# Kernel tuning notes

Measured on AMD Instinct MI355X. Metric: run time of the kernel, lower is better.

The kernel has to match this reference:

```python
import jax, jax.numpy as jnp
import numpy as np

B, C, T, F = 16, 2, 2000, 257

def setup_inputs() -> dict:
    key = jax.random.key(0)
    k1, = jax.random.split(key, 1)
    inp = jax.random.normal(k1, (B, C, T, F, 2), dtype=jnp.float32)
    s_1 = jnp.zeros((B, 1, F, 1), dtype=jnp.float32)
    weights = jnp.ones((1, C, 1, F, 1), dtype=jnp.float32)
    bias = jnp.zeros((1, C, 1, F, 1), dtype=jnp.float32)
    alpha_param = jnp.full((1, 1, F, 1), -4.0, dtype=jnp.float32)
    return {"input": inp, "s_1": s_1, "weights": weights, "bias": bias, "alpha_param": alpha_param}

def reference(input, s_1, weights, bias, alpha_param):
    # input: [B, C, T, F, 2]
    in_data2 = jnp.sum(input ** 2, axis=-1, keepdims=True)       # [B, C, T, F, 1]
    alpha = jax.nn.sigmoid(alpha_param)                           # [1, 1, F, 1]
    x_seq = jnp.moveaxis(in_data2[:, 0:1], 2, 0)                  # [T, B, 1, F, 1]

    def step(s, xt):
        s_new = s * (1.0 - alpha) + xt * alpha                    # [B, 1, F, 1]
        return s_new, s_new

    s_final, smooth = jax.lax.scan(step, s_1, x_seq)              # smooth: [T, B, 1, F, 1]
    smooth_data = jnp.sqrt(jnp.moveaxis(smooth, 0, 2))            # [B, 1, T, F, 1]
    cat_data = jnp.concatenate([smooth_data, jnp.sqrt(in_data2[:, 1:])], axis=1)  # [B, C, T, F, 1]
    res = input / (cat_data + 1e-8) * weights + bias              # [B, C, T, F, 2]
    return res, s_final, smooth_data
```

## Files before the change

### kernel.cpp

```cpp
#include <hip/hip_runtime.h>
#include <math.h>

#define B 16
#define C 2
#define T 2000
#define F 257
#define NC 100
#define L  (T / NC)

#define RES_SIZE   (B * C * T * F * 2)
#define OFF_SFINAL (RES_SIZE)
#define OFF_SMOOTH (RES_SIZE + B * F)

#define N_CARRY (B * NC * F)
#define G0      ((N_CARRY + 255) / 256)
#define SLAB4   (T * F * 2 / 4)
#define N_V4    (B * SLAB4)
#define G1      ((N_V4 + 255) / 256)

__device__ __forceinline__ float sigmoidf_(float x) {
    return 1.0f / (1.0f + expf(-x));
}

__global__ __launch_bounds__(256) void k_phase1(const float* __restrict__ input,
                                                const float* __restrict__ alpha_param,
                                                const float* __restrict__ weights,
                                                const float* __restrict__ bias,
                                                float* __restrict__ carry,
                                                float* __restrict__ out) {
    int bid = blockIdx.x;
    if (bid < G1) {
        int idx = bid * 256 + threadIdx.x;
        if (idx >= N_V4) return;
        int b   = idx / SLAB4;
        int rem = idx - b * SLAB4;

        const float4* ip = (const float4*)(input + ((size_t)(b * C + 1) * T) * F * 2) + rem;
        float4 v = *ip;

        int e  = rem * 2;
        int f0 = e % F;
        int f1 = (f0 + 1 == F) ? 0 : (f0 + 1);

        float w0 = weights[F + f0], w1 = weights[F + f1];
        float q0 = bias[F + f0],    q1 = bias[F + f1];

        float inv0 = 1.0f / (sqrtf(v.x * v.x + v.y * v.y) + 1e-8f);
        float inv1 = 1.0f / (sqrtf(v.z * v.z + v.w * v.w) + 1e-8f);

        float4 rr;
        rr.x = v.x * inv0 * w0 + q0;
        rr.y = v.y * inv0 * w0 + q0;
        rr.z = v.z * inv1 * w1 + q1;
        rr.w = v.w * inv1 * w1 + q1;

        float4* rp = (float4*)(out + ((size_t)(b * C + 1) * T) * F * 2) + rem;
        *rp = rr;
    } else {
        int tid = (bid - G1) * 256 + threadIdx.x;
        if (tid >= N_CARRY) return;
        int f = tid % F;
        int r = tid / F;
        int c = r % NC;
        int b = r / NC;

        float a = sigmoidf_(alpha_param[f]);
        float beta = 1.0f - a;

        const float2* inp = (const float2*)input
                          + ((size_t)(b * C + 0) * T + (size_t)c * L) * F + f;
        float s = 0.0f;
#pragma unroll
        for (int t = 0; t < L; ++t) {
            float2 v = inp[(size_t)t * F];
            s = beta * s + a * (v.x * v.x + v.y * v.y);
        }
        carry[((size_t)b * NC + c) * F + f] = s;
    }
}

__global__ __launch_bounds__(256) void k_phase2(const float* __restrict__ input,
                                                const float* __restrict__ s_1,
                                                const float* __restrict__ alpha_param,
                                                const float* __restrict__ weights,
                                                const float* __restrict__ bias,
                                                const float* __restrict__ carry,
                                                float* __restrict__ out) {
    int tid = blockIdx.x * 256 + threadIdx.x;
    if (tid >= N_CARRY) return;
    int f = tid % F;
    int r = tid / F;
    int c = r % NC;
    int b = r / NC;

    float a = sigmoidf_(alpha_param[f]);
    float beta = 1.0f - a;
    float bL = 1.0f;
#pragma unroll
    for (int i = 0; i < L; ++i) bL *= beta;
    float bL2 = bL * bL;
    float bL3 = bL2 * bL;
    float bL4 = bL2 * bL2;

    const float* cp = carry + (size_t)b * NC * F + f;
    float s = s_1[b * F + f];
    int j = 0;
    for (; j + 4 <= c; j += 4) {
        float c0 = cp[(size_t)(j    ) * F];
        float c1 = cp[(size_t)(j + 1) * F];
        float c2 = cp[(size_t)(j + 2) * F];
        float c3 = cp[(size_t)(j + 3) * F];
        s = fmaf(bL4, s, fmaf(bL3, c0, fmaf(bL2, c1, fmaf(bL, c2, c3))));
    }
    for (; j < c; ++j) s = fmaf(bL, s, cp[(size_t)j * F]);

    float w0 = weights[f];
    float q0 = bias[f];

    const float2* inp = (const float2*)input
                      + ((size_t)(b * C + 0) * T + (size_t)c * L) * F + f;
    float2* res = (float2*)out
                + ((size_t)(b * C + 0) * T + (size_t)c * L) * F + f;
    float* smooth = out + OFF_SMOOTH + ((size_t)b * T + (size_t)c * L) * F + f;

#pragma unroll
    for (int t = 0; t < L; ++t) {
        float2 v = inp[(size_t)t * F];
        float x = v.x * v.x + v.y * v.y;
        s = beta * s + a * x;
        float sm = sqrtf(s);
        float inv = 1.0f / (sm + 1e-8f);
        float2 rr;
        rr.x = v.x * inv * w0 + q0;
        rr.y = v.y * inv * w0 + q0;
        res[(size_t)t * F] = rr;
        smooth[(size_t)t * F] = sm;
    }
    if (c == NC - 1) out[OFF_SFINAL + (size_t)b * F + f] = s;
}

extern "C" void kernel_launch(void* const* d_in, const int* in_sizes, int n_in,
                              void* d_out, int out_size, void* d_ws, size_t ws_size,
                              hipStream_t stream) {
    const float* input       = (const float*)d_in[0];
    const float* s_1         = (const float*)d_in[1];
    const float* weights     = (const float*)d_in[2];
    const float* bias        = (const float*)d_in[3];
    const float* alpha_param = (const float*)d_in[4];
    float* out = (float*)d_out;

    float* carry = (float*)d_ws;

    k_phase1<<<G1 + G0, 256, 0, stream>>>(input, alpha_param, weights, bias, carry, out);
    k_phase2<<<G0, 256, 0, stream>>>(input, s_1, alpha_param, weights, bias, carry, out);
}
```

Baseline: 298.0 us.

## Fuse chunked scan phases into one kernel with shared-memory carry propagation

Replaces the two-kernel chunked scan, which wrote per-chunk carries to global memory, with a single kernel. Each block owns 16 frequencies by 16 time chunks of 125 steps and exchanges chunk carries through shared memory after a block barrier. The channel-1 elementwise normalization blocks run in the same launch. This removes a kernel launch and the global carry round-trip. In exchange there are far fewer threads, each running much longer serial recurrences, so latency hiding and load balance may suffer.

```diff
diff --git a/kernel.cpp b/kernel.cpp
--- a/kernel.cpp
+++ b/kernel.cpp
@@ -5,15 +5,17 @@
 #define C 2
 #define T 2000
 #define F 257
-#define NC 100
-#define L  (T / NC)
 
 #define RES_SIZE   (B * C * T * F * 2)
 #define OFF_SFINAL (RES_SIZE)
 #define OFF_SMOOTH (RES_SIZE + B * F)
 
-#define N_CARRY (B * NC * F)
-#define G0      ((N_CARRY + 255) / 256)
+#define FW 16
+#define TC 16
+#define LW (T / TC)
+#define NFT ((F + FW - 1) / FW)
+#define NCH0 (B * NFT)
+
 #define SLAB4   (T * F * 2 / 4)
 #define N_V4    (B * SLAB4)
 #define G1      ((N_V4 + 255) / 256)
@@ -22,15 +24,70 @@
     return 1.0f / (1.0f + expf(-x));
 }
 
-__global__ __launch_bounds__(256) void k_phase1(const float* __restrict__ input,
-                                                const float* __restrict__ alpha_param,
-                                                const float* __restrict__ weights,
-                                                const float* __restrict__ bias,
-                                                float* __restrict__ carry,
-                                                float* __restrict__ out) {
+__global__ __launch_bounds__(256) void k_all(const float* __restrict__ input,
+                                             const float* __restrict__ s_1,
+                                             const float* __restrict__ alpha_param,
+                                             const float* __restrict__ weights,
+                                             const float* __restrict__ bias,
+                                             float* __restrict__ out) {
     int bid = blockIdx.x;
-    if (bid < G1) {
-        int idx = bid * 256 + threadIdx.x;
+    if (bid < NCH0) {
+        int ft = bid % NFT;
+        int b  = bid / NFT;
+        int tid = threadIdx.x;
+        int f = tid & (FW - 1);
+        int c = tid >> 4;
+        int fg = ft * FW + f;
+        bool act = (fg < F);
+
+        __shared__ float carr[TC][FW + 1];
+
+        float a = 0.0f, beta = 1.0f, s = 0.0f;
+        const float2* base = (const float2*)input;
+        if (act) {
+            a = sigmoidf_(alpha_param[fg]);
+            beta = 1.0f - a;
+            base = (const float2*)input
+                 + ((size_t)(b * C + 0) * T + (size_t)c * LW) * F + fg;
+#pragma unroll 5
+            for (int t = 0; t < LW; ++t) {
+                float2 v = base[(size_t)t * F];
+                s = beta * s + a * (v.x * v.x + v.y * v.y);
+            }
+        }
+        carr[c][f] = s;
+        __syncthreads();
+        if (!act) return;
+
+        float bL = 1.0f;
+        for (int i = 0; i < LW; ++i) bL *= beta;
+
+        float S = s_1[b * F + fg];
+        for (int j = 0; j < c; ++j) S = fmaf(bL, S, carr[j][f]);
+
+        float w0 = weights[fg];
+        float q0 = bias[fg];
+
+        float2* res = (float2*)out
+                    + ((size_t)(b * C + 0) * T + (size_t)c * LW) * F + fg;
+        float* smb = out + OFF_SMOOTH + ((size_t)b * T + (size_t)c * LW) * F + fg;
+
+        s = S;
+#pragma unroll 5
+        for (int t = 0; t < LW; ++t) {
+            float2 v = base[(size_t)t * F];
+            s = beta * s + a * (v.x * v.x + v.y * v.y);
+            float sm = sqrtf(s);
+            float inv = 1.0f / (sm + 1e-8f);
+            float2 rr;
+            rr.x = v.x * inv * w0 + q0;
+            rr.y = v.y * inv * w0 + q0;
+            res[(size_t)t * F] = rr;
+            smb[(size_t)t * F] = sm;
+        }
+        if (c == TC - 1) out[OFF_SFINAL + (size_t)b * F + fg] = s;
+    } else {
+        int idx = (bid - NCH0) * 256 + threadIdx.x;
         if (idx >= N_V4) return;
         int b   = idx / SLAB4;
         int rem = idx - b * SLAB4;
@@ -56,87 +113,7 @@
 
         float4* rp = (float4*)(out + ((size_t)(b * C + 1) * T) * F * 2) + rem;
         *rp = rr;
-    } else {
-        int tid = (bid - G1) * 256 + threadIdx.x;
-        if (tid >= N_CARRY) return;
-        int f = tid % F;
-        int r = tid / F;
-        int c = r % NC;
-        int b = r / NC;
-
-        float a = sigmoidf_(alpha_param[f]);
-        float beta = 1.0f - a;
-
-        const float2* inp = (const float2*)input
-                          + ((size_t)(b * C + 0) * T + (size_t)c * L) * F + f;
-        float s = 0.0f;
-#pragma unroll
-        for (int t = 0; t < L; ++t) {
-            float2 v = inp[(size_t)t * F];
-            s = beta * s + a * (v.x * v.x + v.y * v.y);
-        }
-        carry[((size_t)b * NC + c) * F + f] = s;
     }
-}
-
-__global__ __launch_bounds__(256) void k_phase2(const float* __restrict__ input,
-                                                const float* __restrict__ s_1,
-                                                const float* __restrict__ alpha_param,
-                                                const float* __restrict__ weights,
-                                                const float* __restrict__ bias,
-                                                const float* __restrict__ carry,
-                                                float* __restrict__ out) {
-    int tid = blockIdx.x * 256 + threadIdx.x;
-    if (tid >= N_CARRY) return;
-    int f = tid % F;
-    int r = tid / F;
-    int c = r % NC;
-    int b = r / NC;
-
-    float a = sigmoidf_(alpha_param[f]);
-    float beta = 1.0f - a;
-    float bL = 1.0f;
-#pragma unroll
-    for (int i = 0; i < L; ++i) bL *= beta;
-    float bL2 = bL * bL;
-    float bL3 = bL2 * bL;
-    float bL4 = bL2 * bL2;
-
-    const float* cp = carry + (size_t)b * NC * F + f;
-    float s = s_1[b * F + f];
-    int j = 0;
-    for (; j + 4 <= c; j += 4) {
-        float c0 = cp[(size_t)(j    ) * F];
-        float c1 = cp[(size_t)(j + 1) * F];
-        float c2 = cp[(size_t)(j + 2) * F];
-        float c3 = cp[(size_t)(j + 3) * F];
-        s = fmaf(bL4, s, fmaf(bL3, c0, fmaf(bL2, c1, fmaf(bL, c2, c3))));
-    }
-    for (; j < c; ++j) s = fmaf(bL, s, cp[(size_t)j * F]);
-
-    float w0 = weights[f];
-    float q0 = bias[f];
-
-    const float2* inp = (const float2*)input
-                      + ((size_t)(b * C + 0) * T + (size_t)c * L) * F + f;
-    float2* res = (float2*)out
-                + ((size_t)(b * C + 0) * T + (size_t)c * L) * F + f;
-    float* smooth = out + OFF_SMOOTH + ((size_t)b * T + (size_t)c * L) * F + f;
-
-#pragma unroll
-    for (int t = 0; t < L; ++t) {
-        float2 v = inp[(size_t)t * F];
-        float x = v.x * v.x + v.y * v.y;
-        s = beta * s + a * x;
-        float sm = sqrtf(s);
-        float inv = 1.0f / (sm + 1e-8f);
-        float2 rr;
-        rr.x = v.x * inv * w0 + q0;
-        rr.y = v.y * inv * w0 + q0;
-        res[(size_t)t * F] = rr;
-        smooth[(size_t)t * F] = sm;
-    }
-    if (c == NC - 1) out[OFF_SFINAL + (size_t)b * F + f] = s;
 }
 
 extern "C" void kernel_launch(void* const* d_in, const int* in_sizes, int n_in,
@@ -149,8 +126,5 @@
     const float* alpha_param = (const float*)d_in[4];
     float* out = (float*)d_out;
 
-    float* carry = (float*)d_ws;
-
-    k_phase1<<<G1 + G0, 256, 0, stream>>>(input, alpha_param, weights, bias, carry, out);
-    k_phase2<<<G0, 256, 0, stream>>>(input, s_1, alpha_param, weights, bias, carry, out);
+    k_all<<<NCH0 + G1, 256, 0, stream>>>(input, s_1, alpha_param, weights, bias, out);
 }
```

New measurement: 342.1 us. 14.8% more time.
